# Kernel optimization log

Measured on AMD Instinct MI355X. Metric: run time of the kernel, lower is better.

Reference implementation:

```python
import jax, jax.numpy as jnp
import numpy as np

B, S, HID, NH = 2, 2048, 2048, 16
DH = HID // NH  # 128


def _rope_tables(seq_len, dim, dtype=jnp.float32):
    inv_freq = 1.0 / (10000.0 ** (jnp.arange(0, dim, 2, dtype=jnp.float32) / dim))
    t = jnp.arange(seq_len, dtype=jnp.float32)
    freqs = jnp.einsum('i,j->ij', t, inv_freq)          # [S, dim/2]
    emb = jnp.concatenate([freqs, freqs], axis=-1)       # [S, dim]
    return jnp.cos(emb)[None, None].astype(dtype), jnp.sin(emb)[None, None].astype(dtype)


def _rotate_half(x):
    x1, x2 = x[..., : x.shape[-1] // 2], x[..., x.shape[-1] // 2 :]
    return jnp.concatenate([-x2, x1], axis=-1)


def setup_inputs() -> dict:
    key = jax.random.key(0)
    ks = jax.random.split(key, 6)
    hidden_states = jax.random.normal(ks[0], (B, S, HID), dtype=jnp.float32)
    scale = 1.0 / np.sqrt(HID)
    Wq = jax.random.normal(ks[1], (HID, HID), dtype=jnp.float32) * scale
    Wk = jax.random.normal(ks[2], (HID, HID), dtype=jnp.float32) * scale
    Wv = jax.random.normal(ks[3], (HID, HID), dtype=jnp.float32) * scale
    Wo = jax.random.normal(ks[4], (HID, HID), dtype=jnp.float32) * scale
    bq = jnp.zeros((HID,), jnp.float32)
    bk = jnp.zeros((HID,), jnp.float32)
    bv = jnp.zeros((HID,), jnp.float32)
    bo = jnp.zeros((HID,), jnp.float32)
    # causal additive mask [1,1,S,S]
    causal = jnp.tril(jnp.ones((S, S), dtype=bool))
    attention_mask = jnp.where(causal, 0.0, -1e9).astype(jnp.float32)[None, None]
    return dict(hidden_states=hidden_states, attention_mask=attention_mask,
                Wq=Wq, bq=bq, Wk=Wk, bk=bk, Wv=Wv, bv=bv, Wo=Wo, bo=bo)


def reference(hidden_states, attention_mask, Wq, bq, Wk, bk, Wv, bv, Wo, bo):
    b, s, _ = hidden_states.shape
    # torch Linear: x @ W.T + b
    q = (hidden_states @ Wq.T + bq).reshape(b, s, NH, DH).transpose(0, 2, 1, 3)
    k = (hidden_states @ Wk.T + bk).reshape(b, s, NH, DH).transpose(0, 2, 1, 3)
    v = (hidden_states @ Wv.T + bv).reshape(b, s, NH, DH).transpose(0, 2, 1, 3)
    cos, sin = _rope_tables(s, DH)
    q = q * cos + _rotate_half(q) * sin
    k = k * cos + _rotate_half(k) * sin
    scores = jnp.einsum('bhqd,bhkd->bhqk', q * (DH ** -0.5), k)
    scores = scores + attention_mask
    probs = jax.nn.softmax(scores, axis=-1)  # dropout: eval mode (identity)
    out = jnp.einsum('bhqk,bhkd->bhqd', probs, v)
    out = out.transpose(0, 2, 1, 3).reshape(b, s, HID)
    return out @ Wo.T + bo
```

## Files before the change

### kernel.cpp

```cpp
#include <hip/hip_runtime.h>
#include <hip/hip_bf16.h>
#include <cstdint>
#include <cstddef>

#define BB 2
#define SS 2048
#define HH 2048
#define NHH 16
#define DHH 128

using f32x4  = __attribute__((ext_vector_type(4))) float;
using bf16x8 = __attribute__((ext_vector_type(8))) __bf16;
using bf16x4 = __attribute__((ext_vector_type(4))) __bf16;
using bfloat = __bf16;

__device__ inline void gload_lds16(const void* g, void* l) {
    __builtin_amdgcn_global_load_lds(
        (const __attribute__((address_space(1))) void*)g,
        (__attribute__((address_space(3))) void*)l, 16, 0, 0);
}

__device__ inline f32x4 mfma16(bf16x8 a, bf16x8 b, f32x4 c) {
    return __builtin_amdgcn_mfma_f32_16x16x32_bf16(a, b, c, 0, 0, 0);
}

template <int CTRL>
__device__ inline float dpp_max_step(float x) {
    int y = __builtin_amdgcn_update_dpp(0, __builtin_bit_cast(int, x), CTRL, 0xf, 0xf, false);
    return fmaxf(x, __builtin_bit_cast(float, y));
}
__device__ inline float rowmax16(float x) {
    x = dpp_max_step<0x121>(x);
    x = dpp_max_step<0x122>(x);
    x = dpp_max_step<0x124>(x);
    x = dpp_max_step<0x128>(x);
    return x;
}

__global__ void cvt_bf16(const float* __restrict__ in, bfloat* __restrict__ out, int n4) {
    int i = blockIdx.x * blockDim.x + threadIdx.x;
    if (i >= n4) return;
    float4 v = reinterpret_cast<const float4*>(in)[i];
    bf16x4 o;
    o[0] = (bfloat)v.x; o[1] = (bfloat)v.y; o[2] = (bfloat)v.z; o[3] = (bfloat)v.w;
    reinterpret_cast<bf16x4*>(out)[i] = o;
}

__global__ void rope_table(float* __restrict__ cosT, float* __restrict__ sinT) {
    int i = blockIdx.x * blockDim.x + threadIdx.x;
    if (i >= SS * 64) return;
    int s = i >> 6, j = i & 63;
    float invf = powf(10000.0f, -(float)j / 64.0f);
    float ang = (float)s * invf;
    cosT[i] = cosf(ang);
    sinT[i] = sinf(ang);
}

template <int OUTMODE>
__global__ __launch_bounds__(256, 2)
void gemm_bt(const bfloat* __restrict__ A, const bfloat* __restrict__ Bt,
             const float* __restrict__ bias, void* __restrict__ C,
             int M, int N, int K,
             const float* __restrict__ cosT, const float* __restrict__ sinT) {
    constexpr int BM = 128, BN = 128, BK = 32;
    __shared__ bfloat As[BM * BK];
    __shared__ bfloat Bs[BN * BK];
    const int t = threadIdx.x, w = t >> 6, l = t & 63;
    const int lr = l & 15, lg = l >> 4;
    const int m0 = blockIdx.x * BM, n0 = blockIdx.y * BN;
    const int wm = (w >> 1) * 64;
    const int base = (t & ~63) * 8;

    f32x4 acc[4][4] = {};

    for (int kb = 0; kb < K; kb += BK) {
#pragma unroll
        for (int i = 0; i < 2; i++) {
            int idx = i * 256 + t;
            int r = idx >> 2, k8 = (idx & 3) << 3;
            gload_lds16(A  + (size_t)(m0 + r) * K + kb + k8, As + (i * 2048 + base));
            gload_lds16(Bt + (size_t)(n0 + r) * K + kb + k8, Bs + (i * 2048 + base));
        }
        __syncthreads();
        bf16x8 af[4], bfr[4];
#pragma unroll
        for (int mi = 0; mi < 4; mi++)
            af[mi] = *reinterpret_cast<const bf16x8*>(&As[(wm + mi * 16 + lr) * BK + lg * 8]);
#pragma unroll
        for (int ni = 0; ni < 4; ni++) {
            int cb = (w & 1) * 32 + (ni & 1) * 16 + (ni >> 1) * 64;
            bfr[ni] = *reinterpret_cast<const bf16x8*>(&Bs[(cb + lr) * BK + lg * 8]);
        }
#pragma unroll
        for (int mi = 0; mi < 4; mi++)
#pragma unroll
            for (int ni = 0; ni < 4; ni++)
                acc[mi][ni] = mfma16(af[mi], bfr[ni], acc[mi][ni]);
        __syncthreads();
    }

    if (OUTMODE <= 2) {
#pragma unroll
        for (int mi = 0; mi < 4; mi++) {
            int row = m0 + wm + mi * 16 + lg * 4;
#pragma unroll
            for (int ni = 0; ni < 4; ni++) {
                int cb = (w & 1) * 32 + (ni & 1) * 16 + (ni >> 1) * 64;
                int col = n0 + cb + lr;
                float bv = bias[col];
#pragma unroll
                for (int j = 0; j < 4; j++) {
                    float v = acc[mi][ni][j] + bv;
                    if (OUTMODE == 1) {
                        ((float*)C)[(size_t)(row + j) * N + col] = v;
                    } else if (OUTMODE == 0) {
                        ((bfloat*)C)[(size_t)(row + j) * N + col] = (bfloat)v;
                    } else {
                        int bb = (row + j) >> 11;
                        int s  = (row + j) & (SS - 1);
                        ((bfloat*)C)[((size_t)(bb * HH + col)) * SS + s] = (bfloat)v;
                    }
                }
            }
        }
    } else {
        const float qscale = 0.088388347648318447f;
#pragma unroll
        for (int mi = 0; mi < 4; mi++) {
            int row = m0 + wm + mi * 16 + lg * 4;
#pragma unroll
            for (int ni = 0; ni < 2; ni++) {
                int d = (w & 1) * 32 + ni * 16 + lr;
                int col1 = n0 + d, col2 = col1 + 64;
                float b1 = bias[col1], b2 = bias[col2];
#pragma unroll
                for (int j = 0; j < 4; j++) {
                    int s = (row + j) & (SS - 1);
                    float c  = cosT[s * 64 + d];
                    float sn = sinT[s * 64 + d];
                    float x1 = acc[mi][ni][j] + b1;
                    float x2 = acc[mi][ni + 2][j] + b2;
                    float o1 = x1 * c - x2 * sn;
                    float o2 = x2 * c + x1 * sn;
                    if (OUTMODE == 3) { o1 *= qscale; o2 *= qscale; }
                    ((bfloat*)C)[(size_t)(row + j) * N + col1] = (bfloat)o1;
                    ((bfloat*)C)[(size_t)(row + j) * N + col2] = (bfloat)o2;
                }
            }
        }
    }
}

__global__ __launch_bounds__(256, 2)
void attn_fwd(const bfloat* __restrict__ Q, const bfloat* __restrict__ K,
              const bfloat* __restrict__ Vt, bfloat* __restrict__ O) {
    __shared__ bfloat Ks[2][64 * 128];
    __shared__ bfloat Vs[2][128 * 64];
    __shared__ bfloat Pw[4][16 * 64];

    const int t = threadIdx.x, w = t >> 6, l = t & 63;
    const int lr = l & 15, lg = l >> 4;
    const int swz = (lr & 7) << 4;

    const int f = blockIdx.x;
    const int xcd = f & 7, slot = f >> 3;
    const int bh = xcd + 8 * (slot >> 5);
    const int qidx = 31 - (slot & 31);
    const int b = bh >> 4, h = bh & 15;
    const int q0 = qidx * 64 + w * 16;

    const size_t bo_ = (size_t)b * SS * HH + (size_t)h * DHH;
    const bfloat* Qp = Q + bo_;
    const bfloat* Kp = K + bo_;
    const bfloat* Vp = Vt + (size_t)(b * NHH + h) * DHH * SS;
    bfloat* Op = O + bo_;

    auto stage = [&](int buf, int kv0) {
#pragma unroll
        for (int i = 0; i < 4; i++) {
            int Ub = (i * 4 + w) * 64;
            int U = Ub + l;
            int r = U >> 4;
            int u = (U & 15) ^ (r & 7);
            gload_lds16(Kp + (size_t)(kv0 + r) * HH + u * 8, &Ks[buf][Ub * 8]);
        }
#pragma unroll
        for (int i = 0; i < 4; i++) {
            int Ub = (i * 4 + w) * 64;
            int U = Ub + l;
            int r = U >> 3;
            int u = (U & 7) ^ (r & 7);
            gload_lds16(Vp + (size_t)r * SS + kv0 + u * 8, &Vs[buf][Ub * 8]);
        }
    };

    bf16x8 qf[4];
#pragma unroll
    for (int kt = 0; kt < 4; kt++)
        qf[kt] = *reinterpret_cast<const bf16x8*>(Qp + (size_t)(q0 + lr) * HH + kt * 32 + lg * 8);

    bf16x8 ones;
#pragma unroll
    for (int e = 0; e < 8; e++) ones[e] = (bfloat)1.0f;

    f32x4 o[8] = {};
    f32x4 lsv = {};
    float m[4];
#pragma unroll
    for (int j = 0; j < 4; j++) m[j] = -1e30f;

    const int nkv = qidx + 1;
    stage(0, 0);
    __syncthreads();

    for (int kv = 0; kv < nkv; ++kv) {
        const int cur = kv & 1;
        if (kv + 1 < nkv) stage(cur ^ 1, (kv + 1) * 64);

        const char* KB = (const char*)&Ks[cur][0];
        const char* VB = (const char*)&Vs[cur][0];

        f32x4 sc[4] = {};
        __builtin_amdgcn_s_setprio(1);
#pragma unroll
        for (int kt = 0; kt < 4; kt++) {
            const int col = (kt * 64 + lg * 16);
#pragma unroll
            for (int kb = 0; kb < 4; kb++) {
                bf16x8 kf = *reinterpret_cast<const bf16x8*>(
                    KB + (kb * 16 + lr) * 256 + (col ^ swz));
                sc[kb] = mfma16(qf[kt], kf, sc[kb]);
            }
        }
        __builtin_amdgcn_s_setprio(0);

        const bool diag = (kv == nkv - 1);
        float p[4][4], alpha[4];
        bool ga = false;
#pragma unroll
        for (int j = 0; j < 4; j++) {
            float v0 = sc[0][j], v1 = sc[1][j], v2 = sc[2][j], v3 = sc[3][j];
            if (diag) {
                int qr = q0 + lg * 4 + j;
                int k0 = kv * 64 + lr;
                if (k0      > qr) v0 = -1e30f;
                if (k0 + 16 > qr) v1 = -1e30f;
                if (k0 + 32 > qr) v2 = -1e30f;
                if (k0 + 48 > qr) v3 = -1e30f;
            }
            float mx = rowmax16(fmaxf(fmaxf(v0, v1), fmaxf(v2, v3)));
            bool grow = mx > m[j] + 8.0f;
            float mn = grow ? mx : m[j];
            alpha[j] = grow ? __expf(m[j] - mn) : 1.0f;
            m[j] = mn;
            ga = ga || grow;
            p[0][j] = __expf(v0 - mn);
            p[1][j] = __expf(v1 - mn);
            p[2][j] = __expf(v2 - mn);
            p[3][j] = __expf(v3 - mn);
        }
        if (__any(ga)) {
#pragma unroll
            for (int j = 0; j < 4; j++) {
                lsv[j] *= alpha[j];
#pragma unroll
                for (int nt = 0; nt < 8; nt++) o[nt][j] *= alpha[j];
            }
        }

        char* pwb = (char*)&Pw[w][0];
#pragma unroll
        for (int j = 0; j < 4; j++) {
            int q = lg * 4 + j;
            int qs = (q & 7) << 4;
#pragma unroll
            for (int kb = 0; kb < 4; kb++)
                *(bfloat*)(pwb + q * 128 + ((kb * 32 + lr * 2) ^ qs)) = (bfloat)p[kb][j];
        }
        asm volatile("s_waitcnt lgkmcnt(0)" ::: "memory");
        __builtin_amdgcn_sched_barrier(0);

        const char* pwr = (const char*)&Pw[w][0];
        bf16x8 pa0 = *reinterpret_cast<const bf16x8*>(pwr + lr * 128 + ((lg * 16) ^ swz));
        bf16x8 pa1 = *reinterpret_cast<const bf16x8*>(pwr + lr * 128 + ((64 + lg * 16) ^ swz));
        __builtin_amdgcn_s_setprio(1);
        lsv = mfma16(pa0, ones, lsv);
        lsv = mfma16(pa1, ones, lsv);
#pragma unroll
        for (int nt = 0; nt < 8; nt++) {
            const char* vb = VB + (nt * 16 + lr) * 128;
            bf16x8 vf0 = *reinterpret_cast<const bf16x8*>(vb + ((lg * 16) ^ swz));
            bf16x8 vf1 = *reinterpret_cast<const bf16x8*>(vb + ((64 + lg * 16) ^ swz));
            o[nt] = mfma16(pa0, vf0, o[nt]);
            o[nt] = mfma16(pa1, vf1, o[nt]);
        }
        __builtin_amdgcn_s_setprio(0);
        __syncthreads();
    }

#pragma unroll
    for (int j = 0; j < 4; j++) {
        float inv = 1.0f / lsv[j];
        int row = q0 + lg * 4 + j;
#pragma unroll
        for (int nt = 0; nt < 8; nt++)
            Op[(size_t)row * HH + nt * 16 + lr] = (bfloat)(o[nt][j] * inv);
    }
}

extern "C" void kernel_launch(void* const* d_in, const int* in_sizes, int n_in,
                              void* d_out, int out_size, void* d_ws, size_t ws_size,
                              hipStream_t stream) {
    (void)in_sizes; (void)n_in; (void)out_size; (void)ws_size;
    const float* hs = (const float*)d_in[0];
    const float* Wq = (const float*)d_in[2];
    const float* bq = (const float*)d_in[3];
    const float* Wk = (const float*)d_in[4];
    const float* bk = (const float*)d_in[5];
    const float* Wv = (const float*)d_in[6];
    const float* bv = (const float*)d_in[7];
    const float* Wo = (const float*)d_in[8];
    const float* bo = (const float*)d_in[9];

    char* ws = (char*)d_ws;
    size_t off = 0;
    auto alloc = [&](size_t bytes) { void* p = ws + off; off += (bytes + 255) & ~(size_t)255; return p; };
    const size_t MK = (size_t)BB * SS * HH;
    const size_t NK = (size_t)HH * HH;

    bfloat* Xb  = (bfloat*)alloc(MK * 2);
    bfloat* Wqb = (bfloat*)alloc(NK * 2);
    bfloat* Wkb = (bfloat*)alloc(NK * 2);
    bfloat* Wvb = (bfloat*)alloc(NK * 2);
    bfloat* Wob = (bfloat*)alloc(NK * 2);
    bfloat* Qb  = (bfloat*)alloc(MK * 2);
    bfloat* Kb  = (bfloat*)alloc(MK * 2);
    bfloat* Vtb = (bfloat*)alloc(MK * 2);
    float*  cosT = (float*)alloc((size_t)SS * 64 * 4);
    float*  sinT = (float*)alloc((size_t)SS * 64 * 4);
    bfloat* AOb = Xb;

    cvt_bf16<<<(int)(MK / 4 / 256), 256, 0, stream>>>(hs, Xb, (int)(MK / 4));
    cvt_bf16<<<(int)(NK / 4 / 256), 256, 0, stream>>>(Wq, Wqb, (int)(NK / 4));
    cvt_bf16<<<(int)(NK / 4 / 256), 256, 0, stream>>>(Wk, Wkb, (int)(NK / 4));
    cvt_bf16<<<(int)(NK / 4 / 256), 256, 0, stream>>>(Wv, Wvb, (int)(NK / 4));
    cvt_bf16<<<(int)(NK / 4 / 256), 256, 0, stream>>>(Wo, Wob, (int)(NK / 4));
    rope_table<<<(SS * 64 + 255) / 256, 256, 0, stream>>>(cosT, sinT);

    dim3 gg(BB * SS / 128, HH / 128);
    gemm_bt<3><<<gg, 256, 0, stream>>>(Xb, Wqb, bq, Qb, BB * SS, HH, HH, cosT, sinT);
    gemm_bt<4><<<gg, 256, 0, stream>>>(Xb, Wkb, bk, Kb, BB * SS, HH, HH, cosT, sinT);
    gemm_bt<2><<<gg, 256, 0, stream>>>(Xb, Wvb, bv, Vtb, BB * SS, HH, HH, nullptr, nullptr);

    attn_fwd<<<1024, 256, 0, stream>>>(Qb, Kb, Vtb, AOb);

    gemm_bt<1><<<gg, 256, 0, stream>>>(AOb, Wob, bo, d_out, BB * SS, HH, HH, nullptr, nullptr);
}
```

Baseline: 331.0 us.

## Batch weight casts and QKV GEMMs into single launches; single-buffer attention at occupancy 4

Merges the four weight-conversion launches into one kernel and the three Q/K/V projection GEMMs into one kernel whose grid selects the weight matrix by blockIdx.y. This cuts launch overhead and tail effects and gives each GEMM launch a larger grid. Attention drops LDS double-buffering for a single buffer with a sync each iteration and raises launch bounds to 4 blocks per CU. The aim is more occupancy, at the cost of losing the overlap between loads and compute.

```diff
diff --git a/kernel.cpp b/kernel.cpp
--- a/kernel.cpp
+++ b/kernel.cpp
@@ -44,6 +44,20 @@
     bf16x4 o;
     o[0] = (bfloat)v.x; o[1] = (bfloat)v.y; o[2] = (bfloat)v.z; o[3] = (bfloat)v.w;
     reinterpret_cast<bf16x4*>(out)[i] = o;
+}
+
+__global__ void cvt_bf16_w(const float* __restrict__ s0, const float* __restrict__ s1,
+                           const float* __restrict__ s2, const float* __restrict__ s3,
+                           bfloat* __restrict__ d0, bfloat* __restrict__ d1,
+                           bfloat* __restrict__ d2, bfloat* __restrict__ d3) {
+    int sel = blockIdx.x >> 12;
+    int i = (blockIdx.x & 4095) * 256 + threadIdx.x;
+    const float* s = sel == 0 ? s0 : sel == 1 ? s1 : sel == 2 ? s2 : s3;
+    bfloat* d = sel == 0 ? d0 : sel == 1 ? d1 : sel == 2 ? d2 : d3;
+    float4 v = reinterpret_cast<const float4*>(s)[i];
+    bf16x4 o;
+    o[0] = (bfloat)v.x; o[1] = (bfloat)v.y; o[2] = (bfloat)v.z; o[3] = (bfloat)v.w;
+    reinterpret_cast<bf16x4*>(d)[i] = o;
 }
 
 __global__ void rope_table(float* __restrict__ cosT, float* __restrict__ sinT) {
@@ -56,12 +70,104 @@
     sinT[i] = sinf(ang);
 }
 
-template <int OUTMODE>
 __global__ __launch_bounds__(256, 2)
-void gemm_bt(const bfloat* __restrict__ A, const bfloat* __restrict__ Bt,
-             const float* __restrict__ bias, void* __restrict__ C,
-             int M, int N, int K,
-             const float* __restrict__ cosT, const float* __restrict__ sinT) {
+void gemm_qkv(const bfloat* __restrict__ A,
+              const bfloat* __restrict__ Bq, const bfloat* __restrict__ Bk,
+              const bfloat* __restrict__ Bv,
+              const float* __restrict__ bq, const float* __restrict__ bk,
+              const float* __restrict__ bv,
+              bfloat* __restrict__ Qo, bfloat* __restrict__ Ko, bfloat* __restrict__ Vto,
+              const float* __restrict__ cosT, const float* __restrict__ sinT) {
+    constexpr int BM = 128, BN = 128, BK = 32, K = HH, N = HH;
+    __shared__ bfloat As[BM * BK];
+    __shared__ bfloat Bs[BN * BK];
+    const int t = threadIdx.x, w = t >> 6, l = t & 63;
+    const int lr = l & 15, lg = l >> 4;
+    const int sel = blockIdx.y >> 4;
+    const bfloat* Bt = sel == 0 ? Bq : sel == 1 ? Bk : Bv;
+    const float* bias = sel == 0 ? bq : sel == 1 ? bk : bv;
+    const int m0 = blockIdx.x * BM, n0 = (blockIdx.y & 15) * BN;
+    const int wm = (w >> 1) * 64;
+    const int base = (t & ~63) * 8;
+
+    f32x4 acc[4][4] = {};
+
+    for (int kb = 0; kb < K; kb += BK) {
+#pragma unroll
+        for (int i = 0; i < 2; i++) {
+            int idx = i * 256 + t;
+            int r = idx >> 2, k8 = (idx & 3) << 3;
+            gload_lds16(A  + (size_t)(m0 + r) * K + kb + k8, As + (i * 2048 + base));
+            gload_lds16(Bt + (size_t)(n0 + r) * K + kb + k8, Bs + (i * 2048 + base));
+        }
+        __syncthreads();
+        bf16x8 af[4], bfr[4];
+#pragma unroll
+        for (int mi = 0; mi < 4; mi++)
+            af[mi] = *reinterpret_cast<const bf16x8*>(&As[(wm + mi * 16 + lr) * BK + lg * 8]);
+#pragma unroll
+        for (int ni = 0; ni < 4; ni++) {
+            int cb = (w & 1) * 32 + (ni & 1) * 16 + (ni >> 1) * 64;
+            bfr[ni] = *reinterpret_cast<const bf16x8*>(&Bs[(cb + lr) * BK + lg * 8]);
+        }
+#pragma unroll
+        for (int mi = 0; mi < 4; mi++)
+#pragma unroll
+            for (int ni = 0; ni < 4; ni++)
+                acc[mi][ni] = mfma16(af[mi], bfr[ni], acc[mi][ni]);
+        __syncthreads();
+    }
+
+    if (sel == 2) {
+#pragma unroll
+        for (int mi = 0; mi < 4; mi++) {
+            int row = m0 + wm + mi * 16 + lg * 4;
+#pragma unroll
+            for (int ni = 0; ni < 4; ni++) {
+                int cb = (w & 1) * 32 + (ni & 1) * 16 + (ni >> 1) * 64;
+                int col = n0 + cb + lr;
+                float bv_ = bias[col];
+#pragma unroll
+                for (int j = 0; j < 4; j++) {
+                    float v = acc[mi][ni][j] + bv_;
+                    int bb = (row + j) >> 11;
+                    int s  = (row + j) & (SS - 1);
+                    Vto[((size_t)(bb * HH + col)) * SS + s] = (bfloat)v;
+                }
+            }
+        }
+    } else {
+        bfloat* C = sel == 0 ? Qo : Ko;
+        const float qscale = sel == 0 ? 0.088388347648318447f : 1.0f;
+#pragma unroll
+        for (int mi = 0; mi < 4; mi++) {
+            int row = m0 + wm + mi * 16 + lg * 4;
+#pragma unroll
+            for (int ni = 0; ni < 2; ni++) {
+                int d = (w & 1) * 32 + ni * 16 + lr;
+                int col1 = n0 + d, col2 = col1 + 64;
+                float b1 = bias[col1], b2 = bias[col2];
+#pragma unroll
+                for (int j = 0; j < 4; j++) {
+                    int s = (row + j) & (SS - 1);
+                    float c  = cosT[s * 64 + d];
+                    float sn = sinT[s * 64 + d];
+                    float x1 = acc[mi][ni][j] + b1;
+                    float x2 = acc[mi][ni + 2][j] + b2;
+                    float o1 = (x1 * c - x2 * sn) * qscale;
+                    float o2 = (x2 * c + x1 * sn) * qscale;
+                    C[(size_t)(row + j) * N + col1] = (bfloat)o1;
+                    C[(size_t)(row + j) * N + col2] = (bfloat)o2;
+                }
+            }
+        }
+    }
+}
+
+__global__ __launch_bounds__(256, 2)
+void gemm_out(const bfloat* __restrict__ A, const bfloat* __restrict__ Bt,
+              const float* __restrict__ bias, float* __restrict__ C,
+              int M, int N, int K) {
     constexpr int BM = 128, BN = 128, BK = 32;
     __shared__ bfloat As[BM * BK];
     __shared__ bfloat Bs[BN * BK];
@@ -99,63 +205,26 @@
         __syncthreads();
     }
 
-    if (OUTMODE <= 2) {
-#pragma unroll
-        for (int mi = 0; mi < 4; mi++) {
-            int row = m0 + wm + mi * 16 + lg * 4;
-#pragma unroll
-            for (int ni = 0; ni < 4; ni++) {
-                int cb = (w & 1) * 32 + (ni & 1) * 16 + (ni >> 1) * 64;
-                int col = n0 + cb + lr;
-                float bv = bias[col];
-#pragma unroll
-                for (int j = 0; j < 4; j++) {
-                    float v = acc[mi][ni][j] + bv;
-                    if (OUTMODE == 1) {
-                        ((float*)C)[(size_t)(row + j) * N + col] = v;
-                    } else if (OUTMODE == 0) {
-                        ((bfloat*)C)[(size_t)(row + j) * N + col] = (bfloat)v;
-                    } else {
-                        int bb = (row + j) >> 11;
-                        int s  = (row + j) & (SS - 1);
-                        ((bfloat*)C)[((size_t)(bb * HH + col)) * SS + s] = (bfloat)v;
-                    }
-                }
-            }
-        }
-    } else {
-        const float qscale = 0.088388347648318447f;
-#pragma unroll
-        for (int mi = 0; mi < 4; mi++) {
-            int row = m0 + wm + mi * 16 + lg * 4;
-#pragma unroll
-            for (int ni = 0; ni < 2; ni++) {
-                int d = (w & 1) * 32 + ni * 16 + lr;
-                int col1 = n0 + d, col2 = col1 + 64;
-                float b1 = bias[col1], b2 = bias[col2];
-#pragma unroll
-                for (int j = 0; j < 4; j++) {
-                    int s = (row + j) & (SS - 1);
-                    float c  = cosT[s * 64 + d];
-                    float sn = sinT[s * 64 + d];
-                    float x1 = acc[mi][ni][j] + b1;
-                    float x2 = acc[mi][ni + 2][j] + b2;
-                    float o1 = x1 * c - x2 * sn;
-                    float o2 = x2 * c + x1 * sn;
-                    if (OUTMODE == 3) { o1 *= qscale; o2 *= qscale; }
-                    ((bfloat*)C)[(size_t)(row + j) * N + col1] = (bfloat)o1;
-                    ((bfloat*)C)[(size_t)(row + j) * N + col2] = (bfloat)o2;
-                }
-            }
-        }
-    }
-}
-
-__global__ __launch_bounds__(256, 2)
+#pragma unroll
+    for (int mi = 0; mi < 4; mi++) {
+        int row = m0 + wm + mi * 16 + lg * 4;
+#pragma unroll
+        for (int ni = 0; ni < 4; ni++) {
+            int cb = (w & 1) * 32 + (ni & 1) * 16 + (ni >> 1) * 64;
+            int col = n0 + cb + lr;
+            float bv = bias[col];
+#pragma unroll
+            for (int j = 0; j < 4; j++)
+                C[(size_t)(row + j) * N + col] = acc[mi][ni][j] + bv;
+        }
+    }
+}
+
+__global__ __launch_bounds__(256, 4)
 void attn_fwd(const bfloat* __restrict__ Q, const bfloat* __restrict__ K,
               const bfloat* __restrict__ Vt, bfloat* __restrict__ O) {
-    __shared__ bfloat Ks[2][64 * 128];
-    __shared__ bfloat Vs[2][128 * 64];
+    __shared__ bfloat Ks[64 * 128];
+    __shared__ bfloat Vs[128 * 64];
     __shared__ bfloat Pw[4][16 * 64];
 
     const int t = threadIdx.x, w = t >> 6, l = t & 63;
@@ -175,14 +244,14 @@
     const bfloat* Vp = Vt + (size_t)(b * NHH + h) * DHH * SS;
     bfloat* Op = O + bo_;
 
-    auto stage = [&](int buf, int kv0) {
+    auto stage = [&](int kv0) {
 #pragma unroll
         for (int i = 0; i < 4; i++) {
             int Ub = (i * 4 + w) * 64;
             int U = Ub + l;
             int r = U >> 4;
             int u = (U & 15) ^ (r & 7);
-            gload_lds16(Kp + (size_t)(kv0 + r) * HH + u * 8, &Ks[buf][Ub * 8]);
+            gload_lds16(Kp + (size_t)(kv0 + r) * HH + u * 8, &Ks[Ub * 8]);
         }
 #pragma unroll
         for (int i = 0; i < 4; i++) {
@@ -190,7 +259,7 @@
             int U = Ub + l;
             int r = U >> 3;
             int u = (U & 7) ^ (r & 7);
-            gload_lds16(Vp + (size_t)r * SS + kv0 + u * 8, &Vs[buf][Ub * 8]);
+            gload_lds16(Vp + (size_t)r * SS + kv0 + u * 8, &Vs[Ub * 8]);
         }
     };
 
@@ -210,15 +279,13 @@
     for (int j = 0; j < 4; j++) m[j] = -1e30f;
 
     const int nkv = qidx + 1;
-    stage(0, 0);
-    __syncthreads();
 
     for (int kv = 0; kv < nkv; ++kv) {
-        const int cur = kv & 1;
-        if (kv + 1 < nkv) stage(cur ^ 1, (kv + 1) * 64);
-
-        const char* KB = (const char*)&Ks[cur][0];
-        const char* VB = (const char*)&Vs[cur][0];
+        stage(kv * 64);
+        __syncthreads();
+
+        const char* KB = (const char*)&Ks[0];
+        const char* VB = (const char*)&Vs[0];
 
         f32x4 sc[4] = {};
         __builtin_amdgcn_s_setprio(1);
@@ -341,18 +408,14 @@
     bfloat* AOb = Xb;
 
     cvt_bf16<<<(int)(MK / 4 / 256), 256, 0, stream>>>(hs, Xb, (int)(MK / 4));
-    cvt_bf16<<<(int)(NK / 4 / 256), 256, 0, stream>>>(Wq, Wqb, (int)(NK / 4));
-    cvt_bf16<<<(int)(NK / 4 / 256), 256, 0, stream>>>(Wk, Wkb, (int)(NK / 4));
-    cvt_bf16<<<(int)(NK / 4 / 256), 256, 0, stream>>>(Wv, Wvb, (int)(NK / 4));
-    cvt_bf16<<<(int)(NK / 4 / 256), 256, 0, stream>>>(Wo, Wob, (int)(NK / 4));
+    cvt_bf16_w<<<4 * 4096, 256, 0, stream>>>(Wq, Wk, Wv, Wo, Wqb, Wkb, Wvb, Wob);
     rope_table<<<(SS * 64 + 255) / 256, 256, 0, stream>>>(cosT, sinT);
 
-    dim3 gg(BB * SS / 128, HH / 128);
-    gemm_bt<3><<<gg, 256, 0, stream>>>(Xb, Wqb, bq, Qb, BB * SS, HH, HH, cosT, sinT);
-    gemm_bt<4><<<gg, 256, 0, stream>>>(Xb, Wkb, bk, Kb, BB * SS, HH, HH, cosT, sinT);
-    gemm_bt<2><<<gg, 256, 0, stream>>>(Xb, Wvb, bv, Vtb, BB * SS, HH, HH, nullptr, nullptr);
+    gemm_qkv<<<dim3(BB * SS / 128, 48), 256, 0, stream>>>(
+        Xb, Wqb, Wkb, Wvb, bq, bk, bv, Qb, Kb, Vtb, cosT, sinT);
 
     attn_fwd<<<1024, 256, 0, stream>>>(Qb, Kb, Vtb, AOb);
 
-    gemm_bt<1><<<gg, 256, 0, stream>>>(AOb, Wob, bo, d_out, BB * SS, HH, HH, nullptr, nullptr);
-}
+    gemm_out<<<dim3(BB * SS / 128, HH / 128), 256, 0, stream>>>(
+        AOb, Wob, bo, (float*)d_out, BB * SS, HH, HH);
+}
```

New measurement: 308.8 us. -6.7%, faster.
